# Performance work log

Hardware: AMD Instinct MI355X
Metric: run time of the kernel (lower is better)

Reference implementation:

```python
import jax, jax.numpy as jnp
import numpy as np

N0, N1, B, NY, NU, NH = 512, 512, 256, 64, 64, 512
_W_SCALE = 0.02  # keep 512-step affine recurrence numerically bounded


def setup_inputs() -> dict:
    key = jax.random.key(0)
    ks = jax.random.split(key, 11)
    s = _W_SCALE
    return {
        "Y0": jax.random.normal(ks[0], (N0, B, NY), jnp.float32),
        "U0": jax.random.normal(ks[1], (N0, B, NU), jnp.float32),
        "U1": jax.random.normal(ks[2], (N1, B, NU), jnp.float32),
        "W_enc": jax.random.normal(ks[3], (NH, NH + NY + NU), jnp.float32) * s,
        "b_enc": jax.random.normal(ks[4], (NH,), jnp.float32) * s,
        "W_x2x": jax.random.normal(ks[5], (NH, NH), jnp.float32) * s,
        "b_x2x": jax.random.normal(ks[6], (NH,), jnp.float32) * s,
        "W_dec": jax.random.normal(ks[7], (NH, NH + NU), jnp.float32) * s,
        "b_dec": jax.random.normal(ks[8], (NH,), jnp.float32) * s,
        "W_y": jax.random.normal(ks[9], (NY, NH + NU), jnp.float32) * s,
        "b_y": jax.random.normal(ks[10], (NY,), jnp.float32) * s,
    }


def reference(Y0, U0, U1, W_enc, b_enc, W_x2x, b_x2x, W_dec, b_dec, W_y, b_y):
    # offset compensation (use_offset_compensate=True)
    yOff = Y0[-1]          # [B, Ny]
    uOff = U0[-1]          # [B, Nu]
    Y0c = Y0 - yOff
    U0c = U0 - uOff
    U1c = U1 - uOff

    nb = U0.shape[1]
    nh = W_x2x.shape[0]
    x0 = jnp.zeros((nb, nh), dtype=Y0.dtype)

    # encoder: affine recurrence x <- Linear(cat(x, y, u))
    def enc_step(x, yu):
        y, u = yu
        x = jnp.concatenate([x, y, u], axis=1) @ W_enc.T + b_enc
        return x, None

    x, _ = jax.lax.scan(enc_step, x0, (Y0c, U0c))
    x = x @ W_x2x.T + b_x2x  # x0hat

    # decoder: affine recurrence x <- Linear(cat(x, u)), collect states
    def dec_step(x, u):
        xn = jnp.concatenate([x, u], axis=1) @ W_dec.T + b_dec
        return xn, xn

    _, Xs = jax.lax.scan(dec_step, x, U1c)
    X2 = jnp.concatenate([x[None], Xs], axis=0)        # [N1+1, B, Nh]
    U2 = jnp.concatenate([U0c[-1:], U1c], axis=0)      # [N1+1, B, Nu]

    Yhat2 = jnp.concatenate([X2, U2], axis=-1) @ W_y.T + b_y  # [N1+1, B, Ny]
    return Yhat2 + yOff
```

## Files before the change

kernel.cpp:

```cpp
#include <hip/hip_runtime.h>
#include <hip/hip_bf16.h>

typedef __attribute__((ext_vector_type(8))) short short8;
typedef __attribute__((ext_vector_type(4))) float f32x4;
typedef __attribute__((ext_vector_type(4))) float fl4;

#define DEVI static __device__ __forceinline__

DEVI short f2bs(float f) { __hip_bfloat16 h = __float2bfloat16(f); short s; __builtin_memcpy(&s, &h, 2); return s; }
DEVI float bs2f(short s) { __hip_bfloat16 h; __builtin_memcpy(&h, &s, 2); return __bfloat162float(h); }
DEVI short8 ld8(const short* p) { return *reinterpret_cast<const short8*>(p); }
DEVI void st8(short* p, short8 v) { *reinterpret_cast<short8*>(p) = v; }
DEVI f32x4 MF(short8 a, short8 b, f32x4 c) { return __builtin_amdgcn_mfma_f32_16x16x32_bf16(a, b, c, 0, 0, 0); }
DEVI void glds16(const short* g, short* l) {
  __builtin_amdgcn_global_load_lds((const __attribute__((address_space(1))) void*)g,
                                   (__attribute__((address_space(3))) void*)l, 16, 0, 0);
}
DEVI int xcd_swz(int bid, int nwg) {
  int q = nwg >> 3, r = nwg & 7;
  int x = bid & 7, i = bid >> 3;
  int base = (x < r) ? x*(q+1) : r*(q+1) + (x - r)*q;
  return base + i;
}

constexpr size_t OF_U1CB = 0;
constexpr size_t OF_ZENC = 8388608;
constexpr size_t OF_MATS = 10485760;
constexpr size_t OF_FWST = 16252928;
constexpr size_t OF_FT   = 16777216;
constexpr size_t OF_RWST = 16908288;
constexpr size_t OF_RT   = 17956864;
constexpr size_t OF_CB   = 18481152;
constexpr size_t OF_WDECB= 18554880;
constexpr size_t OF_WYB  = 18849792;
constexpr size_t OF_WX2X = 18886656;
constexpr size_t OF_D8   = 19148800;
constexpr size_t OF_S8   = 28323840;
constexpr size_t OF_XFIN = 36712448;
constexpr size_t OF_X0HAT= 36843520;
constexpr size_t OF_WAUG = 36974592;
constexpr size_t OF_BIAS = 37564416;
constexpr size_t OF_CB3  = 37576704;

enum {
  SL_AD1W=0, SL_AD1T, SL_AD2W, SL_AD2T, SL_AD4W, SL_AD4T, SL_AD8W, SL_AD8T, SL_AD16W, SL_AD16T,
  SL_AE1W, SL_AE1T, SL_AE2W, SL_AE2T, SL_AE4W, SL_AE4T, SL_AE8W, SL_AE8T, SL_AE16W, SL_AE16T,
  SL_QD2W, SL_QE2W
};

DEVI short8 cvt8(const float* p) {
  fl4 a = *(const fl4*)p, b = *(const fl4*)(p + 4);
  short8 v;
  v[0]=f2bs(a[0]); v[1]=f2bs(a[1]); v[2]=f2bs(a[2]); v[3]=f2bs(a[3]);
  v[4]=f2bs(b[0]); v[5]=f2bs(b[1]); v[6]=f2bs(b[2]); v[7]=f2bs(b[3]);
  return v;
}
DEVI short8 sub8(const float* p, const float* o) {
  fl4 a = *(const fl4*)p, b = *(const fl4*)(p + 4);
  fl4 c = *(const fl4*)o, d = *(const fl4*)(o + 4);
  short8 v;
  v[0]=f2bs(a[0]-c[0]); v[1]=f2bs(a[1]-c[1]); v[2]=f2bs(a[2]-c[2]); v[3]=f2bs(a[3]-c[3]);
  v[4]=f2bs(b[0]-d[0]); v[5]=f2bs(b[1]-d[1]); v[6]=f2bs(b[2]-d[2]); v[7]=f2bs(b[3]-d[3]);
  return v;
}
DEVI short8 gath8(const float* p, int stride) {
  short8 v;
#pragma unroll
  for (int e = 0; e < 8; ++e) v[e] = f2bs(p[(size_t)e*stride]);
  return v;
}

__global__ __launch_bounds__(256) void k_prep(
    const float* __restrict__ Y0, const float* __restrict__ U0, const float* __restrict__ U1,
    const float* __restrict__ Wenc, const float* __restrict__ Wdec,
    const float* __restrict__ Wx2x, const float* __restrict__ Wy,
    const float* __restrict__ bdec, const float* __restrict__ benc,
    short* __restrict__ ws)
{
  const size_t total8 = 12341248 / 8;
  for (size_t gidx = (size_t)blockIdx.x*256 + threadIdx.x; gidx < total8; gidx += (size_t)gridDim.x*256) {
    size_t i = gidx * 8;
    short8 v; size_t dst;
    if (i < 8388608) {
      int r = (int)((i >> 6) & 255), u = (int)(i & 63);
      v = sub8(U1 + i, U0 + (size_t)(511*256 + r)*64 + u);
      dst = OF_U1CB + i;
    } else if ((i -= 8388608) < 2097152) {
      int tt = (int)(i >> 15), r = (int)((i >> 7) & 255), z = (int)(i & 127);
      int t = 448 + tt;
      if (z < 64) v = sub8(Y0 + ((size_t)t*256 + r)*64 + z, Y0 + (size_t)(511*256 + r)*64 + z);
      else        v = sub8(U0 + ((size_t)t*256 + r)*64 + (z-64), U0 + (size_t)(511*256 + r)*64 + (z-64));
      dst = OF_ZENC + i;
    } else if ((i -= 2097152) < 262144) {
      v = cvt8(Wdec + (size_t)(i>>9)*576 + (i&511));
      dst = OF_MATS + (size_t)SL_AD1W*262144 + i;
    } else if ((i -= 262144) < 262144) {
      v = gath8(Wdec + (size_t)(i&511)*576 + (i>>9), 576);
      dst = OF_MATS + (size_t)SL_AD1T*262144 + i;
    } else if ((i -= 262144) < 262144) {
      v = cvt8(Wenc + (size_t)(i>>9)*640 + (i&511));
      dst = OF_MATS + (size_t)SL_AE1W*262144 + i;
    } else if ((i -= 262144) < 262144) {
      v = gath8(Wenc + (size_t)(i&511)*640 + (i>>9), 640);
      dst = OF_MATS + (size_t)SL_AE1T*262144 + i;
    } else if ((i -= 262144) < 294912) {
      v = cvt8(Wdec + i);
      dst = OF_WDECB + i;
    } else if ((i -= 294912) < 36864) {
      v = cvt8(Wy + i);
      dst = OF_WYB + i;
    } else if ((i -= 36864) < 262144) {
      v = cvt8(Wx2x + i);
      dst = OF_WX2X + i;
    } else if ((i -= 262144) < 32768) {
      v = gath8(Wdec + (size_t)(i&511)*576 + 512 + (i>>9), 576);
      dst = OF_FT + i;
    } else if ((i -= 32768) < 32768) {
      v = cvt8(Wdec + (size_t)(i>>6)*576 + 512 + (i&63));
      dst = OF_FWST + (size_t)15*32768 + i;
    } else if ((i -= 32768) < 65536) {
      v = gath8(Wenc + (size_t)(i&511)*640 + 512 + (i>>9), 640);
      dst = OF_RT + i;
    } else if ((i -= 65536) < 65536) {
      v = cvt8(Wenc + (size_t)(i>>7)*640 + 512 + (i&127));
      dst = OF_RWST + (size_t)15*65536 + i;
    } else if ((i -= 65536) < 8192) {
      if (i < 512) v = cvt8(bdec + i); else { for (int e = 0; e < 8; ++e) v[e] = 0; }
      dst = OF_CB + i;
    } else {
      i -= 8192;
      if (i < 512) v = cvt8(benc + i); else { for (int e = 0; e < 8; ++e) v[e] = 0; }
      dst = OF_CB + 8192 + i;
    }
    st8(ws + dst, v);
  }
}

struct BItem {
  const short* A; const short* Y; short* C; const void* initp;
  float* outF; const float* yOffp;
  int M, N, lda, ldy, ldc, kd32, initMode, tileStart, nN, Tout, ldInit;
};
struct BBatch { BItem it[36]; int n; int tiles; };

__global__ __launch_bounds__(256) void k_bgemm(BBatch b)
{
  __shared__ short As[2*2048];
  __shared__ short Bs[2*4096];
  const int lbid = xcd_swz((int)blockIdx.x, (int)gridDim.x);
  int ii = 0;
  for (int t = 1; t < b.n; ++t) if (lbid >= b.it[t].tileStart) ii = t;
  BItem g = b.it[ii];
  const int tau = lbid - g.tileStart;
  const int R0 = (tau / g.nN) * 64;
  const int C0 = (tau % g.nN) * 128;
  const int tid = threadIdx.x, lane = tid & 63;
  const int l15 = lane & 15;
  const int kqs = ((lane>>4) ^ ((lane>>1)&3))*8;
  const int w = tid >> 6;
  const int srow = lane >> 2;
  const int scolz = ((lane&3) ^ ((lane>>3)&3))*8;
  f32x4 acc[4][2];
  if (g.initMode == 0) {
#pragma unroll
    for (int rt = 0; rt < 4; ++rt)
#pragma unroll
      for (int ct = 0; ct < 2; ++ct)
#pragma unroll
        for (int e = 0; e < 4; ++e) acc[rt][ct][e] = 0.f;
  } else if (g.initMode == 1) {
    const short* C0p = (const short*)g.initp;
#pragma unroll
    for (int rt = 0; rt < 4; ++rt)
#pragma unroll
      for (int ct = 0; ct < 2; ++ct) {
        int c = C0 + w*32 + ct*16 + l15; if (c >= g.N) c = g.N - 1;
#pragma unroll
        for (int e = 0; e < 4; ++e) {
          int r = R0 + rt*16 + 4*(lane>>4) + e; if (r >= g.M) r = g.M - 1;
          acc[rt][ct][e] = bs2f(C0p[(size_t)r*g.ldInit + c]);
        }
      }
  } else {
    const float* v = (const float*)g.initp;
#pragma unroll
    for (int ct = 0; ct < 2; ++ct) {
      int c = C0 + w*32 + ct*16 + l15; if (c >= g.N) c = g.N - 1;
      float vv = v[c];
#pragma unroll
      for (int rt = 0; rt < 4; ++rt)
#pragma unroll
        for (int e = 0; e < 4; ++e) acc[rt][ct][e] = vv;
    }
  }
  auto stage = [&](int kt, int buf) {
    int kb = kt*32;
    int ra = R0 + w*16 + srow; ra = (ra < g.M) ? ra : g.M - 1;
    glds16(g.A + (size_t)ra*g.lda + kb + scolz, &As[buf*2048 + w*512]);
#pragma unroll
    for (int l = 0; l < 2; ++l) {
      int cb_ = C0 + w*32 + l*16 + srow; cb_ = (cb_ < g.N) ? cb_ : g.N - 1;
      glds16(g.Y + (size_t)cb_*g.ldy + kb + scolz, &Bs[buf*4096 + w*1024 + l*512]);
    }
  };
  if (g.kd32 > 0) {
    stage(0, 0);
    __syncthreads();
    int cur = 0;
    for (int kt = 0; kt < g.kd32; ++kt) {
      if (kt + 1 < g.kd32) stage(kt + 1, cur ^ 1);
      short8 xf[4], yf[2];
#pragma unroll
      for (int rt = 0; rt < 4; ++rt) xf[rt] = ld8(&As[cur*2048 + (rt*16 + l15)*32 + kqs]);
#pragma unroll
      for (int ct = 0; ct < 2; ++ct) yf[ct] = ld8(&Bs[cur*4096 + (w*32 + ct*16 + l15)*32 + kqs]);
#pragma unroll
      for (int ct = 0; ct < 2; ++ct)
#pragma unroll
        for (int rt = 0; rt < 4; ++rt) acc[rt][ct] = MF(xf[rt], yf[ct], acc[rt][ct]);
      __syncthreads();
      cur ^= 1;
    }
  }
  if (g.outF) {
#pragma unroll
    for (int rt = 0; rt < 4; ++rt)
#pragma unroll
      for (int ct = 0; ct < 2; ++ct) {
        int c = C0 + w*32 + ct*16 + l15;
        if (c >= g.N) continue;
#pragma unroll
        for (int e = 0; e < 4; ++e) {
          int r = R0 + rt*16 + 4*(lane>>4) + e;
          if (r < g.M)
            g.outF[((size_t)g.Tout*256 + (r & 255))*64 + c] = acc[rt][ct][e] + g.yOffp[(size_t)(r & 255)*64 + c];
        }
      }
  } else {
#pragma unroll
    for (int rt = 0; rt < 4; ++rt)
#pragma unroll
      for (int ct = 0; ct < 2; ++ct) {
        int c = C0 + w*32 + ct*16 + l15;
        if (c >= g.N) continue;
#pragma unroll
        for (int e = 0; e < 4; ++e) {
          int r = R0 + rt*16 + 4*(lane>>4) + e;
          if (r < g.M) g.C[(size_t)r*g.ldc + c] = f2bs(acc[rt][ct][e]);
        }
      }
  }
}

__global__ __launch_bounds__(256) void k_phase1t(
    const short* __restrict__ u1cb, const short* __restrict__ fwst,
    const short* __restrict__ cbD, short* __restrict__ D,
    const short* __restrict__ zenc, const short* __restrict__ rwst,
    const short* __restrict__ cbE, short* __restrict__ Epart)
{
  __shared__ short As[2*2048];
  __shared__ short Bs[2*4096];
  const int lbid = xcd_swz((int)blockIdx.x, (int)gridDim.x);
  const int tid = threadIdx.x, lane = tid & 63;
  const int l15 = lane & 15;
  const int kqs = ((lane>>4) ^ ((lane>>1)&3))*8;
  const int w = tid >> 6;
  const int srow = lane >> 2;
  const int scolz = ((lane&3) ^ ((lane>>3)&3))*8;
  f32x4 acc[4][2];
  if (lbid < 256) {
    const int bb = lbid;
    const int chunk = bb >> 6;
    const int quarter = (bb >> 4) & 3;
    const int R0 = ((bb >> 2) & 3) * 64;
    const int C0 = (bb & 3) * 128;
#pragma unroll
    for (int ct = 0; ct < 2; ++ct) {
      float vv = (quarter == 0) ? bs2f(cbE[C0 + w*32 + ct*16 + l15]) : 0.f;
#pragma unroll
      for (int rt = 0; rt < 4; ++rt)
#pragma unroll
        for (int e = 0; e < 4; ++e) acc[rt][ct][e] = vv;
    }
    auto stage = [&](int kt, int buf) {
      int j = quarter*4 + (kt >> 2), kb = (kt & 3)*32;
      int ra = R0 + w*16 + srow;
      glds16(zenc + ((size_t)(chunk*16 + j)*256 + ra)*128 + kb + scolz, &As[buf*2048 + w*512]);
#pragma unroll
      for (int l = 0; l < 2; ++l) {
        int cb_ = C0 + w*32 + l*16 + srow;
        glds16(rwst + ((size_t)j*512 + cb_)*128 + kb + scolz, &Bs[buf*4096 + w*1024 + l*512]);
      }
    };
    stage(0, 0);
    __syncthreads();
    int cur = 0;
    for (int kt = 0; kt < 16; ++kt) {
      if (kt < 15) stage(kt + 1, cur ^ 1);
      short8 xf[4], yf[2];
#pragma unroll
      for (int rt = 0; rt < 4; ++rt) xf[rt] = ld8(&As[cur*2048 + (rt*16 + l15)*32 + kqs]);
#pragma unroll
      for (int ct = 0; ct < 2; ++ct) yf[ct] = ld8(&Bs[cur*4096 + (w*32 + ct*16 + l15)*32 + kqs]);
#pragma unroll
      for (int ct = 0; ct < 2; ++ct)
#pragma unroll
        for (int rt = 0; rt < 4; ++rt) acc[rt][ct] = MF(xf[rt], yf[ct], acc[rt][ct]);
      __syncthreads();
      cur ^= 1;
    }
    short* O = Epart + (size_t)(quarter*4 + chunk)*131072;
#pragma unroll
    for (int rt = 0; rt < 4; ++rt)
#pragma unroll
      for (int ct = 0; ct < 2; ++ct) {
        int c = C0 + w*32 + ct*16 + l15;
#pragma unroll
        for (int e = 0; e < 4; ++e) {
          int r = R0 + rt*16 + 4*(lane>>4) + e;
          O[(size_t)r*512 + c] = f2bs(acc[rt][ct][e]);
        }
      }
  } else {
    const int bb = lbid - 256;
    const int chunk = bb >> 4;
    const int R0 = ((bb >> 2) & 3) * 64;
    const int C0 = (bb & 3) * 128;
#pragma unroll
    for (int ct = 0; ct < 2; ++ct) {
      float vv = bs2f(cbD[C0 + w*32 + ct*16 + l15]);
#pragma unroll
      for (int rt = 0; rt < 4; ++rt)
#pragma unroll
        for (int e = 0; e < 4; ++e) acc[rt][ct][e] = vv;
    }
    auto stage = [&](int kt, int buf) {
      int j = kt >> 1, kb = (kt & 1)*32;
      int ra = R0 + w*16 + srow;
      glds16(u1cb + ((size_t)(chunk*8 + j)*256 + ra)*64 + kb + scolz, &As[buf*2048 + w*512]);
#pragma unroll
      for (int l = 0; l < 2; ++l) {
        int cb_ = C0 + w*32 + l*16 + srow;
        glds16(fwst + ((size_t)(8 + j)*512 + cb_)*64 + kb + scolz, &Bs[buf*4096 + w*1024 + l*512]);
      }
    };
    stage(0, 0);
    __syncthreads();
    int cur = 0;
    for (int kt = 0; kt < 16; ++kt) {
      if (kt < 15) stage(kt + 1, cur ^ 1);
      short8 xf[4], yf[2];
#pragma unroll
      for (int rt = 0; rt < 4; ++rt) xf[rt] = ld8(&As[cur*2048 + (rt*16 + l15)*32 + kqs]);
#pragma unroll
      for (int ct = 0; ct < 2; ++ct) yf[ct] = ld8(&Bs[cur*4096 + (w*32 + ct*16 + l15)*32 + kqs]);
#pragma unroll
      for (int ct = 0; ct < 2; ++ct)
#pragma unroll
        for (int rt = 0; rt < 4; ++rt) acc[rt][ct] = MF(xf[rt], yf[ct], acc[rt][ct]);
      __syncthreads();
      cur ^= 1;
    }
#pragma unroll
    for (int rt = 0; rt < 4; ++rt)
#pragma unroll
      for (int ct = 0; ct < 2; ++ct) {
        int c = C0 + w*32 + ct*16 + l15;
#pragma unroll
        for (int e = 0; e < 4; ++e) {
          int r = R0 + rt*16 + 4*(lane>>4) + e;
          D[((size_t)chunk*256 + r)*512 + c] = f2bs(acc[rt][ct][e]);
        }
      }
  }
}

__global__ __launch_bounds__(256) void k_add4(const short* __restrict__ Ep, short* __restrict__ E)
{
  size_t i8 = ((size_t)blockIdx.x*256 + threadIdx.x) * 8;
  int chunk = (int)(i8 >> 17);
  size_t off = i8 & 131071;
  short8 s0 = ld8(Ep + (size_t)(0*4 + chunk)*131072 + off);
  short8 s1 = ld8(Ep + (size_t)(1*4 + chunk)*131072 + off);
  short8 s2 = ld8(Ep + (size_t)(2*4 + chunk)*131072 + off);
  short8 s3 = ld8(Ep + (size_t)(3*4 + chunk)*131072 + off);
  short8 r;
#pragma unroll
  for (int e = 0; e < 8; ++e)
    r[e] = f2bs(bs2f(s0[e]) + bs2f(s1[e]) + bs2f(s2[e]) + bs2f(s3[e]));
  st8(E + (size_t)chunk*131072 + off, r);
}

__global__ __launch_bounds__(256) void k_xstep4(
    const short* __restrict__ A, short* __restrict__ C,
    const short* __restrict__ u1cb, const short* __restrict__ W4,
    const short* __restrict__ bias4, const float* __restrict__ yOff,
    float* __restrict__ out, int m4, int yOnly)
{
  __shared__ short As[2*2048];
  __shared__ short Bs[2*4096];
  const int lbid = xcd_swz((int)blockIdx.x, (int)gridDim.x);
  const int tid = threadIdx.x, lane = tid & 63;
  const int l15 = lane & 15;
  const int kq = 8 * (lane >> 4);
  const int kqs = ((lane>>4) ^ ((lane>>1)&3))*8;
  const int w = tid >> 6;
  const int srow = lane >> 2;
  const int scolz = ((lane&3) ^ ((lane>>3)&3))*8;
  int rtile, ctile;
  if (yOnly) { rtile = lbid >> 1; ctile = 4 + (lbid & 1); }
  else { rtile = lbid / 6; ctile = lbid % 6; }
  const int R0 = rtile * 64, C0 = ctile * 128;
  const int chunk = R0 >> 8;
  f32x4 acc[4][2];
#pragma unroll
  for (int ct = 0; ct < 2; ++ct) {
    float bv = bs2f(bias4[C0 + w*32 + ct*16 + l15]);
#pragma unroll
    for (int rt = 0; rt < 4; ++rt)
#pragma unroll
      for (int e = 0; e < 4; ++e) acc[rt][ct][e] = bv;
  }
  auto stage = [&](int kt, int buf) {
    int kb = kt*32;
    int ra = R0 + w*16 + srow;
    glds16(A + (size_t)ra*512 + kb + scolz, &As[buf*2048 + w*512]);
#pragma unroll
    for (int l = 0; l < 2; ++l) {
      int cb_ = C0 + w*32 + l*16 + srow;
      glds16(W4 + (size_t)cb_*768 + kb + scolz, &Bs[buf*4096 + w*1024 + l*512]);
    }
  };
  stage(0, 0);
  __syncthreads();
  int cur = 0;
  for (int kt = 0; kt < 16; ++kt) {
    if (kt < 15) stage(kt + 1, cur ^ 1);
    short8 xf[4], yf[2];
#pragma unroll
    for (int rt = 0; rt < 4; ++rt) xf[rt] = ld8(&As[cur*2048 + (rt*16 + l15)*32 + kqs]);
#pragma unroll
    for (int ct = 0; ct < 2; ++ct) yf[ct] = ld8(&Bs[cur*4096 + (w*32 + ct*16 + l15)*32 + kqs]);
#pragma unroll
    for (int ct = 0; ct < 2; ++ct)
#pragma unroll
      for (int rt = 0; rt < 4; ++rt) acc[rt][ct] = MF(xf[rt], yf[ct], acc[rt][ct]);
    __syncthreads();
    cur ^= 1;
  }
#pragma unroll
  for (int kk2 = 0; kk2 < 8; ++kk2) {
    int dt = kk2 >> 1, uo = (kk2 & 1)*32 + kq;
    short8 uf[4], yf[2];
#pragma unroll
    for (int rt = 0; rt < 4; ++rt) {
      int ur = (chunk*8 + 4*m4 + dt)*256 + ((R0 + rt*16 + l15) & 255);
      uf[rt] = ld8(u1cb + (size_t)ur*64 + uo);
    }
#pragma unroll
    for (int ct = 0; ct < 2; ++ct)
      yf[ct] = ld8(W4 + (size_t)(C0 + w*32 + ct*16 + l15)*768 + 512 + kk2*32 + kq);
#pragma unroll
    for (int ct = 0; ct < 2; ++ct)
#pragma unroll
      for (int rt = 0; rt < 4; ++rt) acc[rt][ct] = MF(uf[rt], yf[ct], acc[rt][ct]);
  }
  if (ctile < 4) {
#pragma unroll
    for (int rt = 0; rt < 4; ++rt)
#pragma unroll
      for (int ct = 0; ct < 2; ++ct) {
        int c = C0 + w*32 + ct*16 + l15;
#pragma unroll
        for (int e = 0; e < 4; ++e) {
          int r = R0 + rt*16 + 4*(lane>>4) + e;
          C[(size_t)r*512 + c] = f2bs(acc[rt][ct][e]);
        }
      }
  } else {
#pragma unroll
    for (int rt = 0; rt < 4; ++rt)
#pragma unroll
      for (int ct = 0; ct < 2; ++ct) {
        int oc = C0 - 512 + w*32 + ct*16 + l15;
        int T = 8*chunk + 4*m4 + 1 + (oc >> 6);
        int col = oc & 63;
#pragma unroll
        for (int e = 0; e < 4; ++e) {
          int rb_ = (R0 + rt*16 + 4*(lane>>4) + e) & 255;
          out[((size_t)T*256 + rb_)*64 + col] = acc[rt][ct][e] + yOff[(size_t)rb_*64 + col];
        }
      }
  }
}

extern "C" void kernel_launch(void* const* d_in, const int* in_sizes, int n_in,
                              void* d_out, int out_size, void* d_ws, size_t ws_size,
                              hipStream_t stream)
{
  const float* Y0   = (const float*)d_in[0];
  const float* U0   = (const float*)d_in[1];
  const float* U1   = (const float*)d_in[2];
  const float* Wenc = (const float*)d_in[3];
  const float* benc = (const float*)d_in[4];
  const float* Wx2x = (const float*)d_in[5];
  const float* bx2x = (const float*)d_in[6];
  const float* Wdec = (const float*)d_in[7];
  const float* bdec = (const float*)d_in[8];
  const float* Wy   = (const float*)d_in[9];
  const float* by   = (const float*)d_in[10];
  float* out = (float*)d_out;
  short* ws = (short*)d_ws;
  const float* yOff = Y0 + (size_t)511*256*64;

  auto MAT = [&](int s) -> short* { return ws + OF_MATS + (size_t)s*262144; };
  auto FTp = [&](int p) -> short* { return ws + OF_FT   + (size_t)p*32768; };
  auto FWs = [&](int j) -> short* { return ws + OF_FWST + (size_t)j*32768; };
  auto RTp = [&](int p) -> short* { return ws + OF_RT   + (size_t)p*65536; };
  auto RWs = [&](int j) -> short* { return ws + OF_RWST + (size_t)j*65536; };
  short* CBB   = ws + OF_CB;
  short* CBEB  = ws + OF_CB + 8192;
  short* CB2   = ws + OF_CB + 2*8192;
  short* CB4   = ws + OF_CB + 3*8192;
  short* CB8   = ws + OF_CB + 4*8192;
  short* CBE2  = ws + OF_CB + 5*8192;
  short* CBE4  = ws + OF_CB + 6*8192;
  short* CBE8  = ws + OF_CB + 7*8192;
  short* CBE16 = ws + OF_CB + 8*8192;
  short* CB3   = ws + OF_CB3;
  short* D8 = ws + OF_D8;
  short* S8 = ws + OF_S8;
  short* WYB = ws + OF_WYB;
  short* W4 = ws + OF_WAUG;
  short* biasb = ws + OF_BIAS;
  short* RX  = W4;
  short* RY1 = W4 + (size_t)512*768;
  short* RY2 = W4 + (size_t)576*768;
  short* RY3 = W4 + (size_t)640*768;
  short* RY4 = W4 + (size_t)704*768;
  auto D8s = [&](int s) -> short* { return D8 + (size_t)s*131072; };
  auto S8s = [&](int s) -> short* { return S8 + (size_t)s*131072; };

  auto addB = [](BBatch& b, const short* A, const short* Y, short* C,
                 int M, int N, int lda, int ldy, int ldc, int im, const void* ip,
                 int ldInit, int kd32) {
    int nN = (N + 127) / 128;
    BItem g{A, Y, C, ip, nullptr, nullptr, M, N, lda, ldy, ldc, kd32, im, b.tiles, nN, 0, ldInit};
    b.it[b.n++] = g; b.tiles += ((M + 63) / 64) * nN;
  };
  auto addSq = [&](BBatch& b, int cs, int xs_, int ys) {
    addB(b, MAT(xs_), MAT(ys), MAT(cs), 512, 512, 512, 512, 512, 0, nullptr, 0, 16);
  };
  auto addFw = [&](BBatch& b, int pq, int wq, int ftp) {
    addB(b, MAT(wq), FTp(ftp), FWs(15 - pq), 512, 64, 512, 512, 64, 0, nullptr, 0, 16);
  };
  auto addFt = [&](BBatch& b, int pdst, int psrc, int wq) {
    addB(b, FTp(psrc), MAT(wq), FTp(pdst), 64, 512, 512, 512, 512, 0, nullptr, 0, 16);
  };
  auto addRw = [&](BBatch& b, int pq, int wq, int rtp) {
    addB(b, MAT(wq), RTp(rtp), RWs(15 - pq), 512, 128, 512, 512, 128, 0, nullptr, 0, 16);
  };
  auto addRt = [&](BBatch& b, int pdst, int psrc, int wq) {
    addB(b, RTp(psrc), MAT(wq), RTp(pdst), 128, 512, 512, 512, 512, 0, nullptr, 0, 16);
  };
  auto addCb = [&](BBatch& b, short* dst, const short* src, int wq) {
    addB(b, src, MAT(wq), dst, 16, 512, 512, 512, 512, 1, src, 512, 16);
  };
  auto addCopy = [&](BBatch& b, const short* src, int ldSrc, short* dst, int M, int N) {
    addB(b, src, src, dst, M, N, ldSrc, ldSrc, 768, 1, src, ldSrc, 0);
  };
  auto addZero = [&](BBatch& b, short* dst, int M, int N) {
    addB(b, WYB, WYB, dst, M, N, 576, 576, 768, 0, nullptr, 0, 0);
  };

  k_prep<<<2048, 256, 0, stream>>>(Y0, U0, U1, Wenc, Wdec, Wx2x, Wy, bdec, benc, ws);

  { BBatch b{}; b.n = 0; b.tiles = 0;
    addSq(b, SL_AD2W, SL_AD1W, SL_AD1T); addSq(b, SL_AD2T, SL_AD1T, SL_AD1W);
    addSq(b, SL_AE2W, SL_AE1W, SL_AE1T); addSq(b, SL_AE2T, SL_AE1T, SL_AE1W);
    addFw(b, 1, SL_AD1W, 0); addFt(b, 1, 0, SL_AD1W);
    addRw(b, 1, SL_AE1W, 0); addRt(b, 1, 0, SL_AE1W);
    addCb(b, CB2, CBB, SL_AD1W); addCb(b, CBE2, CBEB, SL_AE1W);
    k_bgemm<<<b.tiles, 256, 0, stream>>>(b); }

  { BBatch b{}; b.n = 0; b.tiles = 0;
    addSq(b, SL_AD4W, SL_AD2W, SL_AD2T); addSq(b, SL_AD4T, SL_AD2T, SL_AD2W);
    addSq(b, SL_AE4W, SL_AE2W, SL_AE2T); addSq(b, SL_AE4T, SL_AE2T, SL_AE2W);
    addFw(b, 2, SL_AD2W, 0); addFw(b, 3, SL_AD2W, 1);
    addFt(b, 2, 0, SL_AD2W); addFt(b, 3, 1, SL_AD2W);
    addRw(b, 2, SL_AE2W, 0); addRw(b, 3, SL_AE2W, 1);
    addRt(b, 2, 0, SL_AE2W); addRt(b, 3, 1, SL_AE2W);
    addCb(b, CB4, CB2, SL_AD2W); addCb(b, CBE4, CBE2, SL_AE2W);
    k_bgemm<<<b.tiles, 256, 0, stream>>>(b); }

  { BBatch b{}; b.n = 0; b.tiles = 0;
    addSq(b, SL_AD8W, SL_AD4W, SL_AD4T); addSq(b, SL_AD8T, SL_AD4T, SL_AD4W);
    addSq(b, SL_AE8W, SL_AE4W, SL_AE4T); addSq(b, SL_AE8T, SL_AE4T, SL_AE4W);
    for (int p = 0; p < 4; ++p) addFw(b, 4 + p, SL_AD4W, p);
    for (int p = 0; p < 4; ++p) { addRw(b, 4 + p, SL_AE4W, p); addRt(b, 4 + p, p, SL_AE4W); }
    addCb(b, CB8, CB4, SL_AD4W);
    addCb(b, CBE8, CBE4, SL_AE4W);
    k_bgemm<<<b.tiles, 256, 0, stream>>>(b); }

  { BBatch b{}; b.n = 0; b.tiles = 0;
    addSq(b, SL_AD16W, SL_AD8W, SL_AD8T); addSq(b, SL_AD16T, SL_AD8T, SL_AD8W);
    addSq(b, SL_AE16W, SL_AE8W, SL_AE8T); addSq(b, SL_AE16T, SL_AE8T, SL_AE8W);
    for (int p = 0; p < 8; ++p) addRw(b, 8 + p, SL_AE8W, p);
    addCb(b, CBE16, CBE8, SL_AE8W);
    k_bgemm<<<b.tiles, 256, 0, stream>>>(b); }

  { BBatch b{}; b.n = 0; b.tiles = 0;
    addSq(b, SL_QD2W, SL_AD16W, SL_AD16T);
    addSq(b, SL_QE2W, SL_AE16W, SL_AE16T);
    addB(b, WYB, MAT(SL_AD1T), RY1, 64, 512, 576, 512, 768, 0, nullptr, 0, 16);
    addB(b, WYB, MAT(SL_AD2T), RY2, 64, 512, 576, 512, 768, 0, nullptr, 0, 16);
    addB(b, WYB, FTp(0), RY1 + 512, 64, 64, 576, 512, 768, 1, WYB + 512, 576, 16);
    addB(b, CBB, MAT(SL_AD2W), CB3, 16, 512, 512, 512, 512, 1, CB2, 512, 16);
    addCopy(b, MAT(SL_AD4W), 512, RX, 512, 512);
    addCopy(b, FWs(12), 64, RX + 512, 512, 64);
    addCopy(b, FWs(13), 64, RX + 576, 512, 64);
    addCopy(b, FWs(14), 64, RX + 640, 512, 64);
    addCopy(b, FWs(15), 64, RX + 704, 512, 64);
    addZero(b, RY1 + 576, 64, 192);
    addZero(b, RY2 + 640, 64, 128);
    addZero(b, RY3 + 704, 64, 64);
    addCopy(b, CB4, 512, biasb, 16, 512);
    addB(b, CBB, WYB, biasb + 512, 16, 64, 512, 576, 768, 2, (const void*)by, 0, 16);
    addB(b, CB2, WYB, biasb + 576, 16, 64, 512, 576, 768, 2, (const void*)by, 0, 16);
    k_bgemm<<<b.tiles, 256, 0, stream>>>(b); }

  { BBatch b{}; b.n = 0; b.tiles = 0;
    addB(b, RY2, MAT(SL_AD1T), RY3, 64, 512, 768, 512, 768, 0, nullptr, 0, 16);
    addB(b, RY2, MAT(SL_AD2T), RY4, 64, 512, 768, 512, 768, 0, nullptr, 0, 16);
    addB(b, RY1, FTp(0), RY2 + 512, 64, 64, 768, 512, 768, 0, nullptr, 0, 16);
    addB(b, RY2, FTp(0), RY3 + 512, 64, 64, 768, 512, 768, 0, nullptr, 0, 16);
    addB(b, CB3, WYB, biasb + 640, 16, 64, 512, 576, 768, 2, (const void*)by, 0, 16);
    addB(b, CB4, WYB, biasb + 704, 16, 64, 512, 576, 768, 2, (const void*)by, 0, 16);
    k_bgemm<<<b.tiles, 256, 0, stream>>>(b); }

  { BBatch b{}; b.n = 0; b.tiles = 0;
    addB(b, RY3, FTp(0), RY4 + 512, 64, 64, 768, 512, 768, 0, nullptr, 0, 16);
    addCopy(b, RY1 + 512, 768, RY2 + 576, 64, 64);
    addCopy(b, RY1 + 512, 768, RY3 + 640, 64, 64);
    addCopy(b, RY1 + 512, 768, RY4 + 704, 64, 64);
    addCopy(b, RY2 + 512, 768, RY3 + 576, 64, 64);
    addCopy(b, RY2 + 512, 768, RY4 + 640, 64, 64);
    addCopy(b, RY3 + 512, 768, RY4 + 576, 64, 64);
    k_bgemm<<<b.tiles, 256, 0, stream>>>(b); }

  k_phase1t<<<1280, 256, 0, stream>>>(ws + OF_U1CB, ws + OF_FWST, CB8, D8,
                                      ws + OF_ZENC, ws + OF_RWST, CBE16, S8);

  k_add4<<<256, 256, 0, stream>>>(S8, D8s(64));

  { BBatch b{}; b.n = 0; b.tiles = 0;
    for (int m = 0; m < 32; ++m)
      addB(b, D8s(2*m), MAT(SL_AD8W), S8s(2*m+1), 256, 512, 512, 512, 512, 1, D8s(2*m+1), 512, 16);
    for (int i = 0; i < 2; ++i)
      addB(b, D8s(64+2*i), MAT(SL_AE16W), D8s(68+i), 256, 512, 512, 512, 512, 1, D8s(64+2*i+1), 512, 16);
    k_bgemm<<<b.tiles, 256, 0, stream>>>(b); }

  { BBatch b{}; b.n = 0; b.tiles = 0;
    for (int i = 0; i < 16; ++i)
      addB(b, S8s(4*i+1), MAT(SL_AD16W), S8s(4*i+2), 256, 512, 512, 512, 512, 1, S8s(4*i+3), 512, 16);
    addB(b, D8s(68), MAT(SL_QE2W), ws + OF_XFIN, 256, 512, 512, 512, 512, 1, D8s(69), 512, 16);
    k_bgemm<<<b.tiles, 256, 0, stream>>>(b); }

  { BBatch b{}; b.n = 0; b.tiles = 0;
    addB(b, ws + OF_XFIN, ws + OF_WX2X, ws + OF_X0HAT, 256, 512, 512, 512, 512, 2, (const void*)bx2x, 0, 16);
    k_bgemm<<<b.tiles, 256, 0, stream>>>(b); }

  { BBatch b{}; b.n = 0; b.tiles = 0;
    addB(b, ws + OF_X0HAT, MAT(SL_QD2W), S8s(0), 256, 512, 512, 512, 512, 1, ws + OF_X0HAT, 512, 0);
    addB(b, ws + OF_X0HAT, MAT(SL_QD2W), S8s(4), 256, 512, 512, 512, 512, 1, S8s(2), 512, 16);
    for (int i = 2; i < 16; ++i)
      addB(b, S8s(4*i-6), MAT(SL_QD2W), S8s(4*i), 256, 512, 512, 512, 512, 1, S8s(4*i-2), 512, 16);
    k_bgemm<<<b.tiles, 256, 0, stream>>>(b); }

  { BBatch b{}; b.n = 0; b.tiles = 0;
    for (int i = 0; i < 16; ++i)
      addB(b, S8s(4*i), MAT(SL_AD16W), S8s(4*i+2), 256, 512, 512, 512, 512, 1, S8s(4*i+1), 512, 16);
    k_bgemm<<<b.tiles, 256, 0, stream>>>(b); }

  { BBatch b{}; b.n = 0; b.tiles = 0;
    for (int j = 0; j < 32; ++j)
      addB(b, S8s(2*j), MAT(SL_AD8W), S8s(2*j+1), 256, 512, 512, 512, 512, 1, D8s(2*j), 512, 16);
    { BItem g{ws + OF_X0HAT, WYB, nullptr, (const void*)by, out, yOff,
              256, 64, 512, 576, 64, 16, 2, b.tiles, 1, 0, 0};
      b.it[b.n++] = g; b.tiles += 4; }
    k_bgemm<<<b.tiles, 256, 0, stream>>>(b); }

  short* Xcur = ws + OF_D8;
  k_xstep4<<<1536, 256, 0, stream>>>(S8, Xcur, ws + OF_U1CB, W4, biasb, yOff, out, 0, 0);
  k_xstep4<<<512, 256, 0, stream>>>(Xcur, nullptr, ws + OF_U1CB, W4, biasb, yOff, out, 1, 1);

  (void)in_sizes; (void)n_in; (void)out_size; (void)ws_size;
}
```

Baseline: 293.6 us.

## Double K-tile depth to 64 in all GEMM kernels and drop x0hat copy

Every MFMA GEMM loop (batched GEMM, phase1, xstep) now stages 64-wide K slices per buffer instead of 32, with a new 8-way XOR swizzle for LDS, and runs two MFMA sub-steps per barrier. This halves the number of __syncthreads and staging rounds per tile, at the cost of doubling LDS use per block, which may lower occupancy. Separately, x0hat is written straight into S8s(0), which removes the identity copy GEMM item that previously moved X0HAT into S8s(0).

```diff
diff --git a/kernel.cpp b/kernel.cpp
--- a/kernel.cpp
+++ b/kernel.cpp
@@ -139,14 +139,14 @@
 struct BItem {
   const short* A; const short* Y; short* C; const void* initp;
   float* outF; const float* yOffp;
-  int M, N, lda, ldy, ldc, kd32, initMode, tileStart, nN, Tout, ldInit;
+  int M, N, lda, ldy, ldc, kd64, initMode, tileStart, nN, Tout, ldInit;
 };
 struct BBatch { BItem it[36]; int n; int tiles; };
 
 __global__ __launch_bounds__(256) void k_bgemm(BBatch b)
 {
-  __shared__ short As[2*2048];
-  __shared__ short Bs[2*4096];
+  __shared__ short As[2*4096];
+  __shared__ short Bs[2*8192];
   const int lbid = xcd_swz((int)blockIdx.x, (int)gridDim.x);
   int ii = 0;
   for (int t = 1; t < b.n; ++t) if (lbid >= b.it[t].tileStart) ii = t;
@@ -156,10 +156,9 @@
   const int C0 = (tau % g.nN) * 128;
   const int tid = threadIdx.x, lane = tid & 63;
   const int l15 = lane & 15;
-  const int kqs = ((lane>>4) ^ ((lane>>1)&3))*8;
   const int w = tid >> 6;
-  const int srow = lane >> 2;
-  const int scolz = ((lane&3) ^ ((lane>>3)&3))*8;
+  const int srow8 = lane >> 3;
+  const int scol8 = ((lane&7) ^ ((lane>>3)&7))*8;
   f32x4 acc[4][2];
   if (g.initMode == 0) {
 #pragma unroll
@@ -194,30 +193,37 @@
     }
   }
   auto stage = [&](int kt, int buf) {
-    int kb = kt*32;
-    int ra = R0 + w*16 + srow; ra = (ra < g.M) ? ra : g.M - 1;
-    glds16(g.A + (size_t)ra*g.lda + kb + scolz, &As[buf*2048 + w*512]);
+    int kb = kt*64;
 #pragma unroll
     for (int l = 0; l < 2; ++l) {
-      int cb_ = C0 + w*32 + l*16 + srow; cb_ = (cb_ < g.N) ? cb_ : g.N - 1;
-      glds16(g.Y + (size_t)cb_*g.ldy + kb + scolz, &Bs[buf*4096 + w*1024 + l*512]);
-    }
-  };
-  if (g.kd32 > 0) {
+      int ra = R0 + w*16 + l*8 + srow8; ra = (ra < g.M) ? ra : g.M - 1;
+      glds16(g.A + (size_t)ra*g.lda + kb + scol8, &As[buf*4096 + (w*16 + l*8)*64]);
+    }
+#pragma unroll
+    for (int l = 0; l < 4; ++l) {
+      int cb_ = C0 + w*32 + l*8 + srow8; cb_ = (cb_ < g.N) ? cb_ : g.N - 1;
+      glds16(g.Y + (size_t)cb_*g.ldy + kb + scol8, &Bs[buf*8192 + (w*32 + l*8)*64]);
+    }
+  };
+  if (g.kd64 > 0) {
     stage(0, 0);
     __syncthreads();
     int cur = 0;
-    for (int kt = 0; kt < g.kd32; ++kt) {
-      if (kt + 1 < g.kd32) stage(kt + 1, cur ^ 1);
-      short8 xf[4], yf[2];
-#pragma unroll
-      for (int rt = 0; rt < 4; ++rt) xf[rt] = ld8(&As[cur*2048 + (rt*16 + l15)*32 + kqs]);
-#pragma unroll
-      for (int ct = 0; ct < 2; ++ct) yf[ct] = ld8(&Bs[cur*4096 + (w*32 + ct*16 + l15)*32 + kqs]);
-#pragma unroll
-      for (int ct = 0; ct < 2; ++ct)
-#pragma unroll
-        for (int rt = 0; rt < 4; ++rt) acc[rt][ct] = MF(xf[rt], yf[ct], acc[rt][ct]);
+    for (int kt = 0; kt < g.kd64; ++kt) {
+      if (kt + 1 < g.kd64) stage(kt + 1, cur ^ 1);
+#pragma unroll
+      for (int kk2 = 0; kk2 < 2; ++kk2) {
+        int pos8 = (((lane>>4) | (kk2<<2)) ^ (lane&7))*8;
+        short8 xf[4], yf[2];
+#pragma unroll
+        for (int rt = 0; rt < 4; ++rt) xf[rt] = ld8(&As[cur*4096 + (rt*16 + l15)*64 + pos8]);
+#pragma unroll
+        for (int ct = 0; ct < 2; ++ct) yf[ct] = ld8(&Bs[cur*8192 + (w*32 + ct*16 + l15)*64 + pos8]);
+#pragma unroll
+        for (int ct = 0; ct < 2; ++ct)
+#pragma unroll
+          for (int rt = 0; rt < 4; ++rt) acc[rt][ct] = MF(xf[rt], yf[ct], acc[rt][ct]);
+      }
       __syncthreads();
       cur ^= 1;
     }
@@ -258,15 +264,14 @@
     const short* __restrict__ zenc, const short* __restrict__ rwst,
     const short* __restrict__ cbE, short* __restrict__ Epart)
 {
-  __shared__ short As[2*2048];
-  __shared__ short Bs[2*4096];
+  __shared__ short As[2*4096];
+  __shared__ short Bs[2*8192];
   const int lbid = xcd_swz((int)blockIdx.x, (int)gridDim.x);
   const int tid = threadIdx.x, lane = tid & 63;
   const int l15 = lane & 15;
-  const int kqs = ((lane>>4) ^ ((lane>>1)&3))*8;
   const int w = tid >> 6;
-  const int srow = lane >> 2;
-  const int scolz = ((lane&3) ^ ((lane>>3)&3))*8;
+  const int srow8 = lane >> 3;
+  const int scol8 = ((lane&7) ^ ((lane>>3)&7))*8;
   f32x4 acc[4][2];
   if (lbid < 256) {
     const int bb = lbid;
@@ -283,29 +288,36 @@
         for (int e = 0; e < 4; ++e) acc[rt][ct][e] = vv;
     }
     auto stage = [&](int kt, int buf) {
-      int j = quarter*4 + (kt >> 2), kb = (kt & 3)*32;
-      int ra = R0 + w*16 + srow;
-      glds16(zenc + ((size_t)(chunk*16 + j)*256 + ra)*128 + kb + scolz, &As[buf*2048 + w*512]);
+      int j = quarter*4 + (kt >> 1), kb = (kt & 1)*64;
 #pragma unroll
       for (int l = 0; l < 2; ++l) {
-        int cb_ = C0 + w*32 + l*16 + srow;
-        glds16(rwst + ((size_t)j*512 + cb_)*128 + kb + scolz, &Bs[buf*4096 + w*1024 + l*512]);
+        int ra = R0 + w*16 + l*8 + srow8;
+        glds16(zenc + ((size_t)(chunk*16 + j)*256 + ra)*128 + kb + scol8, &As[buf*4096 + (w*16 + l*8)*64]);
+      }
+#pragma unroll
+      for (int l = 0; l < 4; ++l) {
+        int cb_ = C0 + w*32 + l*8 + srow8;
+        glds16(rwst + ((size_t)j*512 + cb_)*128 + kb + scol8, &Bs[buf*8192 + (w*32 + l*8)*64]);
       }
     };
     stage(0, 0);
     __syncthreads();
     int cur = 0;
-    for (int kt = 0; kt < 16; ++kt) {
-      if (kt < 15) stage(kt + 1, cur ^ 1);
-      short8 xf[4], yf[2];
-#pragma unroll
-      for (int rt = 0; rt < 4; ++rt) xf[rt] = ld8(&As[cur*2048 + (rt*16 + l15)*32 + kqs]);
-#pragma unroll
-      for (int ct = 0; ct < 2; ++ct) yf[ct] = ld8(&Bs[cur*4096 + (w*32 + ct*16 + l15)*32 + kqs]);
-#pragma unroll
-      for (int ct = 0; ct < 2; ++ct)
-#pragma unroll
-        for (int rt = 0; rt < 4; ++rt) acc[rt][ct] = MF(xf[rt], yf[ct], acc[rt][ct]);
+    for (int kt = 0; kt < 8; ++kt) {
+      if (kt < 7) stage(kt + 1, cur ^ 1);
+#pragma unroll
+      for (int kk2 = 0; kk2 < 2; ++kk2) {
+        int pos8 = (((lane>>4) | (kk2<<2)) ^ (lane&7))*8;
+        short8 xf[4], yf[2];
+#pragma unroll
+        for (int rt = 0; rt < 4; ++rt) xf[rt] = ld8(&As[cur*4096 + (rt*16 + l15)*64 + pos8]);
+#pragma unroll
+        for (int ct = 0; ct < 2; ++ct) yf[ct] = ld8(&Bs[cur*8192 + (w*32 + ct*16 + l15)*64 + pos8]);
+#pragma unroll
+        for (int ct = 0; ct < 2; ++ct)
+#pragma unroll
+          for (int rt = 0; rt < 4; ++rt) acc[rt][ct] = MF(xf[rt], yf[ct], acc[rt][ct]);
+      }
       __syncthreads();
       cur ^= 1;
     }
@@ -335,29 +347,36 @@
         for (int e = 0; e < 4; ++e) acc[rt][ct][e] = vv;
     }
     auto stage = [&](int kt, int buf) {
-      int j = kt >> 1, kb = (kt & 1)*32;
-      int ra = R0 + w*16 + srow;
-      glds16(u1cb + ((size_t)(chunk*8 + j)*256 + ra)*64 + kb + scolz, &As[buf*2048 + w*512]);
+      int j = kt;
 #pragma unroll
       for (int l = 0; l < 2; ++l) {
-        int cb_ = C0 + w*32 + l*16 + srow;
-        glds16(fwst + ((size_t)(8 + j)*512 + cb_)*64 + kb + scolz, &Bs[buf*4096 + w*1024 + l*512]);
+        int ra = R0 + w*16 + l*8 + srow8;
+        glds16(u1cb + ((size_t)(chunk*8 + j)*256 + ra)*64 + scol8, &As[buf*4096 + (w*16 + l*8)*64]);
+      }
+#pragma unroll
+      for (int l = 0; l < 4; ++l) {
+        int cb_ = C0 + w*32 + l*8 + srow8;
+        glds16(fwst + ((size_t)(8 + j)*512 + cb_)*64 + scol8, &Bs[buf*8192 + (w*32 + l*8)*64]);
       }
     };
     stage(0, 0);
     __syncthreads();
     int cur = 0;
-    for (int kt = 0; kt < 16; ++kt) {
-      if (kt < 15) stage(kt + 1, cur ^ 1);
-      short8 xf[4], yf[2];
-#pragma unroll
-      for (int rt = 0; rt < 4; ++rt) xf[rt] = ld8(&As[cur*2048 + (rt*16 + l15)*32 + kqs]);
-#pragma unroll
-      for (int ct = 0; ct < 2; ++ct) yf[ct] = ld8(&Bs[cur*4096 + (w*32 + ct*16 + l15)*32 + kqs]);
-#pragma unroll
-      for (int ct = 0; ct < 2; ++ct)
-#pragma unroll
-        for (int rt = 0; rt < 4; ++rt) acc[rt][ct] = MF(xf[rt], yf[ct], acc[rt][ct]);
+    for (int kt = 0; kt < 8; ++kt) {
+      if (kt < 7) stage(kt + 1, cur ^ 1);
+#pragma unroll
+      for (int kk2 = 0; kk2 < 2; ++kk2) {
+        int pos8 = (((lane>>4) | (kk2<<2)) ^ (lane&7))*8;
+        short8 xf[4], yf[2];
+#pragma unroll
+        for (int rt = 0; rt < 4; ++rt) xf[rt] = ld8(&As[cur*4096 + (rt*16 + l15)*64 + pos8]);
+#pragma unroll
+        for (int ct = 0; ct < 2; ++ct) yf[ct] = ld8(&Bs[cur*8192 + (w*32 + ct*16 + l15)*64 + pos8]);
+#pragma unroll
+        for (int ct = 0; ct < 2; ++ct)
+#pragma unroll
+          for (int rt = 0; rt < 4; ++rt) acc[rt][ct] = MF(xf[rt], yf[ct], acc[rt][ct]);
+      }
       __syncthreads();
       cur ^= 1;
     }
@@ -397,16 +416,15 @@
     const short* __restrict__ bias4, const float* __restrict__ yOff,
     float* __restrict__ out, int m4, int yOnly)
 {
-  __shared__ short As[2*2048];
-  __shared__ short Bs[2*4096];
+  __shared__ short As[2*4096];
+  __shared__ short Bs[2*8192];
   const int lbid = xcd_swz((int)blockIdx.x, (int)gridDim.x);
   const int tid = threadIdx.x, lane = tid & 63;
   const int l15 = lane & 15;
   const int kq = 8 * (lane >> 4);
-  const int kqs = ((lane>>4) ^ ((lane>>1)&3))*8;
   const int w = tid >> 6;
-  const int srow = lane >> 2;
-  const int scolz = ((lane&3) ^ ((lane>>3)&3))*8;
+  const int srow8 = lane >> 3;
+  const int scol8 = ((lane&7) ^ ((lane>>3)&7))*8;
   int rtile, ctile;
   if (yOnly) { rtile = lbid >> 1; ctile = 4 + (lbid & 1); }
   else { rtile = lbid / 6; ctile = lbid % 6; }
@@ -422,29 +440,36 @@
       for (int e = 0; e < 4; ++e) acc[rt][ct][e] = bv;
   }
   auto stage = [&](int kt, int buf) {
-    int kb = kt*32;
-    int ra = R0 + w*16 + srow;
-    glds16(A + (size_t)ra*512 + kb + scolz, &As[buf*2048 + w*512]);
+    int kb = kt*64;
 #pragma unroll
     for (int l = 0; l < 2; ++l) {
-      int cb_ = C0 + w*32 + l*16 + srow;
-      glds16(W4 + (size_t)cb_*768 + kb + scolz, &Bs[buf*4096 + w*1024 + l*512]);
+      int ra = R0 + w*16 + l*8 + srow8;
+      glds16(A + (size_t)ra*512 + kb + scol8, &As[buf*4096 + (w*16 + l*8)*64]);
+    }
+#pragma unroll
+    for (int l = 0; l < 4; ++l) {
+      int cb_ = C0 + w*32 + l*8 + srow8;
+      glds16(W4 + (size_t)cb_*768 + kb + scol8, &Bs[buf*8192 + (w*32 + l*8)*64]);
     }
   };
   stage(0, 0);
   __syncthreads();
   int cur = 0;
-  for (int kt = 0; kt < 16; ++kt) {
-    if (kt < 15) stage(kt + 1, cur ^ 1);
-    short8 xf[4], yf[2];
-#pragma unroll
-    for (int rt = 0; rt < 4; ++rt) xf[rt] = ld8(&As[cur*2048 + (rt*16 + l15)*32 + kqs]);
-#pragma unroll
-    for (int ct = 0; ct < 2; ++ct) yf[ct] = ld8(&Bs[cur*4096 + (w*32 + ct*16 + l15)*32 + kqs]);
-#pragma unroll
-    for (int ct = 0; ct < 2; ++ct)
-#pragma unroll
-      for (int rt = 0; rt < 4; ++rt) acc[rt][ct] = MF(xf[rt], yf[ct], acc[rt][ct]);
+  for (int kt = 0; kt < 8; ++kt) {
+    if (kt < 7) stage(kt + 1, cur ^ 1);
+#pragma unroll
+    for (int kk2 = 0; kk2 < 2; ++kk2) {
+      int pos8 = (((lane>>4) | (kk2<<2)) ^ (lane&7))*8;
+      short8 xf[4], yf[2];
+#pragma unroll
+      for (int rt = 0; rt < 4; ++rt) xf[rt] = ld8(&As[cur*4096 + (rt*16 + l15)*64 + pos8]);
+#pragma unroll
+      for (int ct = 0; ct < 2; ++ct) yf[ct] = ld8(&Bs[cur*8192 + (w*32 + ct*16 + l15)*64 + pos8]);
+#pragma unroll
+      for (int ct = 0; ct < 2; ++ct)
+#pragma unroll
+        for (int rt = 0; rt < 4; ++rt) acc[rt][ct] = MF(xf[rt], yf[ct], acc[rt][ct]);
+    }
     __syncthreads();
     cur ^= 1;
   }
@@ -543,28 +568,28 @@
 
   auto addB = [](BBatch& b, const short* A, const short* Y, short* C,
                  int M, int N, int lda, int ldy, int ldc, int im, const void* ip,
-                 int ldInit, int kd32) {
+                 int ldInit, int kd64) {
     int nN = (N + 127) / 128;
-    BItem g{A, Y, C, ip, nullptr, nullptr, M, N, lda, ldy, ldc, kd32, im, b.tiles, nN, 0, ldInit};
+    BItem g{A, Y, C, ip, nullptr, nullptr, M, N, lda, ldy, ldc, kd64, im, b.tiles, nN, 0, ldInit};
     b.it[b.n++] = g; b.tiles += ((M + 63) / 64) * nN;
   };
   auto addSq = [&](BBatch& b, int cs, int xs_, int ys) {
-    addB(b, MAT(xs_), MAT(ys), MAT(cs), 512, 512, 512, 512, 512, 0, nullptr, 0, 16);
+    addB(b, MAT(xs_), MAT(ys), MAT(cs), 512, 512, 512, 512, 512, 0, nullptr, 0, 8);
   };
   auto addFw = [&](BBatch& b, int pq, int wq, int ftp) {
-    addB(b, MAT(wq), FTp(ftp), FWs(15 - pq), 512, 64, 512, 512, 64, 0, nullptr, 0, 16);
+    addB(b, MAT(wq), FTp(ftp), FWs(15 - pq), 512, 64, 512, 512, 64, 0, nullptr, 0, 8);
   };
   auto addFt = [&](BBatch& b, int pdst, int psrc, int wq) {
-    addB(b, FTp(psrc), MAT(wq), FTp(pdst), 64, 512, 512, 512, 512, 0, nullptr, 0, 16);
+    addB(b, FTp(psrc), MAT(wq), FTp(pdst), 64, 512, 512, 512, 512, 0, nullptr, 0, 8);
   };
   auto addRw = [&](BBatch& b, int pq, int wq, int rtp) {
-    addB(b, MAT(wq), RTp(rtp), RWs(15 - pq), 512, 128, 512, 512, 128, 0, nullptr, 0, 16);
+    addB(b, MAT(wq), RTp(rtp), RWs(15 - pq), 512, 128, 512, 512, 128, 0, nullptr, 0, 8);
   };
   auto addRt = [&](BBatch& b, int pdst, int psrc, int wq) {
-    addB(b, RTp(psrc), MAT(wq), RTp(pdst), 128, 512, 512, 512, 512, 0, nullptr, 0, 16);
+    addB(b, RTp(psrc), MAT(wq), RTp(pdst), 128, 512, 512, 512, 512, 0, nullptr, 0, 8);
   };
   auto addCb = [&](BBatch& b, short* dst, const short* src, int wq) {
-    addB(b, src, MAT(wq), dst, 16, 512, 512, 512, 512, 1, src, 512, 16);
+    addB(b, src, MAT(wq), dst, 16, 512, 512, 512, 512, 1, src, 512, 8);
   };
   auto addCopy = [&](BBatch& b, const short* src, int ldSrc, short* dst, int M, int N) {
     addB(b, src, src, dst, M, N, ldSrc, ldSrc, 768, 1, src, ldSrc, 0);
@@ -612,10 +637,10 @@
   { BBatch b{}; b.n = 0; b.tiles = 0;
     addSq(b, SL_QD2W, SL_AD16W, SL_AD16T);
     addSq(b, SL_QE2W, SL_AE16W, SL_AE16T);
-    addB(b, WYB, MAT(SL_AD1T), RY1, 64, 512, 576, 512, 768, 0, nullptr, 0, 16);
-    addB(b, WYB, MAT(SL_AD2T), RY2, 64, 512, 576, 512, 768, 0, nullptr, 0, 16);
-    addB(b, WYB, FTp(0), RY1 + 512, 64, 64, 576, 512, 768, 1, WYB + 512, 576, 16);
-    addB(b, CBB, MAT(SL_AD2W), CB3, 16, 512, 512, 512, 512, 1, CB2, 512, 16);
+    addB(b, WYB, MAT(SL_AD1T), RY1, 64, 512, 576, 512, 768, 0, nullptr, 0, 8);
+    addB(b, WYB, MAT(SL_AD2T), RY2, 64, 512, 576, 512, 768, 0, nullptr, 0, 8);
+    addB(b, WYB, FTp(0), RY1 + 512, 64, 64, 576, 512, 768, 1, WYB + 512, 576, 8);
+    addB(b, CBB, MAT(SL_AD2W), CB3, 16, 512, 512, 512, 512, 1, CB2, 512, 8);
     addCopy(b, MAT(SL_AD4W), 512, RX, 512, 512);
     addCopy(b, FWs(12), 64, RX + 512, 512, 64);
     addCopy(b, FWs(13), 64, RX + 576, 512, 64);
@@ -625,21 +650,21 @@
     addZero(b, RY2 + 640, 64, 128);
     addZero(b, RY3 + 704, 64, 64);
     addCopy(b, CB4, 512, biasb, 16, 512);
-    addB(b, CBB, WYB, biasb + 512, 16, 64, 512, 576, 768, 2, (const void*)by, 0, 16);
-    addB(b, CB2, WYB, biasb + 576, 16, 64, 512, 576, 768, 2, (const void*)by, 0, 16);
-    k_bgemm<<<b.tiles, 256, 0, stream>>>(b); }
-
-  { BBatch b{}; b.n = 0; b.tiles = 0;
-    addB(b, RY2, MAT(SL_AD1T), RY3, 64, 512, 768, 512, 768, 0, nullptr, 0, 16);
-    addB(b, RY2, MAT(SL_AD2T), RY4, 64, 512, 768, 512, 768, 0, nullptr, 0, 16);
-    addB(b, RY1, FTp(0), RY2 + 512, 64, 64, 768, 512, 768, 0, nullptr, 0, 16);
-    addB(b, RY2, FTp(0), RY3 + 512, 64, 64, 768, 512, 768, 0, nullptr, 0, 16);
-    addB(b, CB3, WYB, biasb + 640, 16, 64, 512, 576, 768, 2, (const void*)by, 0, 16);
-    addB(b, CB4, WYB, biasb + 704, 16, 64, 512, 576, 768, 2, (const void*)by, 0, 16);
-    k_bgemm<<<b.tiles, 256, 0, stream>>>(b); }
-
-  { BBatch b{}; b.n = 0; b.tiles = 0;
-    addB(b, RY3, FTp(0), RY4 + 512, 64, 64, 768, 512, 768, 0, nullptr, 0, 16);
+    addB(b, CBB, WYB, biasb + 512, 16, 64, 512, 576, 768, 2, (const void*)by, 0, 8);
+    addB(b, CB2, WYB, biasb + 576, 16, 64, 512, 576, 768, 2, (const void*)by, 0, 8);
+    k_bgemm<<<b.tiles, 256, 0, stream>>>(b); }
+
+  { BBatch b{}; b.n = 0; b.tiles = 0;
+    addB(b, RY2, MAT(SL_AD1T), RY3, 64, 512, 768, 512, 768, 0, nullptr, 0, 8);
+    addB(b, RY2, MAT(SL_AD2T), RY4, 64, 512, 768, 512, 768, 0, nullptr, 0, 8);
+    addB(b, RY1, FTp(0), RY2 + 512, 64, 64, 768, 512, 768, 0, nullptr, 0, 8);
+    addB(b, RY2, FTp(0), RY3 + 512, 64, 64, 768, 512, 768, 0, nullptr, 0, 8);
+    addB(b, CB3, WYB, biasb + 640, 16, 64, 512, 576, 768, 2, (const void*)by, 0, 8);
+    addB(b, CB4, WYB, biasb + 704, 16, 64, 512, 576, 768, 2, (const void*)by, 0, 8);
+    k_bgemm<<<b.tiles, 256, 0, stream>>>(b); }
+
+  { BBatch b{}; b.n = 0; b.tiles = 0;
+    addB(b, RY3, FTp(0), RY4 + 512, 64, 64, 768, 512, 768, 0, nullptr, 0, 8);
     addCopy(b, RY1 + 512, 768, RY2 + 576, 64, 64);
     addCopy(b, RY1 + 512, 768, RY3 + 640, 64, 64);
     addCopy(b, RY1 + 512, 768, RY4 + 704, 64, 64);
@@ -655,38 +680,37 @@
 
   { BBatch b{}; b.n = 0; b.tiles = 0;
     for (int m = 0; m < 32; ++m)
-      addB(b, D8s(2*m), MAT(SL_AD8W), S8s(2*m+1), 256, 512, 512, 512, 512, 1, D8s(2*m+1), 512, 16);
+      addB(b, D8s(2*m), MAT(SL_AD8W), S8s(2*m+1), 256, 512, 512, 512, 512, 1, D8s(2*m+1), 512, 8);
     for (int i = 0; i < 2; ++i)
-      addB(b, D8s(64+2*i), MAT(SL_AE16W), D8s(68+i), 256, 512, 512, 512, 512, 1, D8s(64+2*i+1), 512, 16);
+      addB(b, D8s(64+2*i), MAT(SL_AE16W), D8s(68+i), 256, 512, 512, 512, 512, 1, D8s(64+2*i+1), 512, 8);
     k_bgemm<<<b.tiles, 256, 0, stream>>>(b); }
 
   { BBatch b{}; b.n = 0; b.tiles = 0;
     for (int i = 0; i < 16; ++i)
-      addB(b, S8s(4*i+1), MAT(SL_AD16W), S8s(4*i+2), 256, 512, 512, 512, 512, 1, S8s(4*i+3), 512, 16);
-    addB(b, D8s(68), MAT(SL_QE2W), ws + OF_XFIN, 256, 512, 512, 512, 512, 1, D8s(69), 512, 16);
-    k_bgemm<<<b.tiles, 256, 0, stream>>>(b); }
-
-  { BBatch b{}; b.n = 0; b.tiles = 0;
-    addB(b, ws + OF_XFIN, ws + OF_WX2X, ws + OF_X0HAT, 256, 512, 512, 512, 512, 2, (const void*)bx2x, 0, 16);
-    k_bgemm<<<b.tiles, 256, 0, stream>>>(b); }
-
-  { BBatch b{}; b.n = 0; b.tiles = 0;
-    addB(b, ws + OF_X0HAT, MAT(SL_QD2W), S8s(0), 256, 512, 512, 512, 512, 1, ws + OF_X0HAT, 512, 0);
-    addB(b, ws + OF_X0HAT, MAT(SL_QD2W), S8s(4), 256, 512, 512, 512, 512, 1, S8s(2), 512, 16);
+      addB(b, S8s(4*i+1), MAT(SL_AD16W), S8s(4*i+2), 256, 512, 512, 512, 512, 1, S8s(4*i+3), 512, 8);
+    addB(b, D8s(68), MAT(SL_QE2W), ws + OF_XFIN, 256, 512, 512, 512, 512, 1, D8s(69), 512, 8);
+    k_bgemm<<<b.tiles, 256, 0, stream>>>(b); }
+
+  { BBatch b{}; b.n = 0; b.tiles = 0;
+    addB(b, ws + OF_XFIN, ws + OF_WX2X, S8s(0), 256, 512, 512, 512, 512, 2, (const void*)bx2x, 0, 8);
+    k_bgemm<<<b.tiles, 256, 0, stream>>>(b); }
+
+  { BBatch b{}; b.n = 0; b.tiles = 0;
+    addB(b, S8s(0), MAT(SL_QD2W), S8s(4), 256, 512, 512, 512, 512, 1, S8s(2), 512, 8);
     for (int i = 2; i < 16; ++i)
-      addB(b, S8s(4*i-6), MAT(SL_QD2W), S8s(4*i), 256, 512, 512, 512, 512, 1, S8s(4*i-2), 512, 16);
+      addB(b, S8s(4*i-6), MAT(SL_QD2W), S8s(4*i), 256, 512, 512, 512, 512, 1, S8s(4*i-2), 512, 8);
     k_bgemm<<<b.tiles, 256, 0, stream>>>(b); }
 
   { BBatch b{}; b.n = 0; b.tiles = 0;
     for (int i = 0; i < 16; ++i)
-      addB(b, S8s(4*i), MAT(SL_AD16W), S8s(4*i+2), 256, 512, 512, 512, 512, 1, S8s(4*i+1), 512, 16);
+      addB(b, S8s(4*i), MAT(SL_AD16W), S8s(4*i+2), 256, 512, 512, 512, 512, 1, S8s(4*i+1), 512, 8);
     k_bgemm<<<b.tiles, 256, 0, stream>>>(b); }
 
   { BBatch b{}; b.n = 0; b.tiles = 0;
     for (int j = 0; j < 32; ++j)
-      addB(b, S8s(2*j), MAT(SL_AD8W), S8s(2*j+1), 256, 512, 512, 512, 512, 1, D8s(2*j), 512, 16);
-    { BItem g{ws + OF_X0HAT, WYB, nullptr, (const void*)by, out, yOff,
-              256, 64, 512, 576, 64, 16, 2, b.tiles, 1, 0, 0};
+      addB(b, S8s(2*j), MAT(SL_AD8W), S8s(2*j+1), 256, 512, 512, 512, 512, 1, D8s(2*j), 512, 8);
+    { BItem g{S8s(0), WYB, nullptr, (const void*)by, out, yOff,
+              256, 64, 512, 576, 64, 8, 2, b.tiles, 1, 0, 0};
       b.it[b.n++] = g; b.tiles += 4; }
     k_bgemm<<<b.tiles, 256, 0, stream>>>(b); }
 
```

Measured after the change: 274.2 us. 1.07x faster.
